# Performance work log

Hardware: AMD Instinct MI355X
Metric: run time of the kernel (lower is better)

Reference implementation:

```python
import jax, jax.numpy as jnp
import numpy as np

N_NODES = 50000
N_EDGES = 600000
N_RELS = 19
D_IN = 128
D_HID = 64
D_OUT = 2


def setup_inputs() -> dict:
    key = jax.random.key(0)
    ks = jax.random.split(key, 10)
    feat = jax.random.normal(ks[0], (N_NODES, D_IN), dtype=jnp.float32)
    src = jax.random.randint(ks[1], (N_EDGES,), 0, N_NODES)
    dst = jax.random.randint(ks[2], (N_EDGES,), 0, N_NODES)
    etype = jax.random.randint(ks[3], (N_EDGES,), 0, N_RELS)
    s1 = 1.0 / np.sqrt(D_IN)
    s2 = 1.0 / np.sqrt(D_HID)
    W1 = jax.random.normal(ks[4], (N_RELS, D_IN, D_HID), dtype=jnp.float32) * s1
    loop1 = jax.random.normal(ks[5], (D_IN, D_HID), dtype=jnp.float32) * s1
    b1 = jnp.zeros((D_HID,), dtype=jnp.float32)
    W2 = jax.random.normal(ks[6], (N_RELS, D_HID, D_OUT), dtype=jnp.float32) * s2
    loop2 = jax.random.normal(ks[7], (D_HID, D_OUT), dtype=jnp.float32) * s2
    b2 = jnp.zeros((D_OUT,), dtype=jnp.float32)
    return {"feat": feat, "W1": W1, "loop1": loop1, "b1": b1,
            "W2": W2, "loop2": loop2, "b2": b2,
            "src": src, "dst": dst, "etype": etype}


def _rel_graph_conv(h, W, loop_w, bias, src, dst, etype, activation):
    # Per-relation transform of all nodes: [N, R, O]; then gather per edge.
    # (num_rels * out_feat is small, so this is cheaper than gathering W per edge.)
    transformed = jnp.einsum('nd,rdo->nro', h, W)
    msg = transformed[src, etype]                      # [E, O] edge messages
    agg = jax.ops.segment_sum(msg, dst, num_segments=h.shape[0])  # scatter-add
    out = agg + h @ loop_w + bias                      # self-loop + bias
    if activation is not None:
        out = activation(out)
    return out


def reference(feat, W1, loop1, b1, W2, loop2, b2, src, dst, etype):
    h = _rel_graph_conv(feat, W1, loop1, b1, src, dst, etype, jax.nn.relu)
    h = _rel_graph_conv(h, W2, loop2, b2, src, dst, etype, None)
    return h
```

## Files before the change

kernel.cpp:

```cpp
#include <hip/hip_runtime.h>

#define N_NODES 50000
#define N_EDGES 600000
#define N_RELS  19
#define D_IN    128
#define D_HID   64
#define D_OUT   2

typedef unsigned short u16;
typedef unsigned int   u32;
typedef __attribute__((ext_vector_type(8))) short sfrag;
typedef __attribute__((ext_vector_type(4))) float f32x4;

__device__ __forceinline__ u16 f2bf(float f){
  union { float f; u32 i; } v; v.f = f;
  u32 r = v.i + 0x7fffu + ((v.i >> 16) & 1u);
  return (u16)(r >> 16);
}

__global__ void k_prep(const float* __restrict__ W1, const float* __restrict__ loop1,
                       const float* __restrict__ W2,
                       u16* __restrict__ W1Tb, u16* __restrict__ loop1Tb,
                       u16* __restrict__ W2Tb){
  int idx = blockIdx.x * 256 + threadIdx.x;
  const int T1 = N_RELS * D_HID * D_IN;
  const int T2 = T1 + N_RELS * 16 * D_HID;
  const int T3 = T2 + D_HID * D_IN;
  if (idx < T1) {
    int r = idx / (D_HID * D_IN);
    int t = idx - r * (D_HID * D_IN);
    int j = t >> 7, d = t & 127;
    W1Tb[idx] = f2bf(W1[(r * D_IN + d) * D_HID + j]);
  } else if (idx < T2) {
    int k2 = idx - T1;
    int r = k2 / (16 * D_HID);
    int t = k2 - r * (16 * D_HID);
    int n = t >> 6, k = t & 63;
    W2Tb[k2] = (n < D_OUT) ? f2bf(W2[(r * D_HID + k) * D_OUT + n]) : (u16)0;
  } else if (idx < T3) {
    int k2 = idx - T2;
    int j = k2 >> 7, d = k2 & 127;
    loop1Tb[k2] = f2bf(loop1[d * D_HID + j]);
  }
}

__global__ void k_zero(int* __restrict__ hist){
  if (threadIdx.x < N_RELS) hist[threadIdx.x] = 0;
}

__global__ __launch_bounds__(256) void k_hist(const int* __restrict__ et, int* __restrict__ hist){
  __shared__ int lh[N_RELS];
  int tid = threadIdx.x;
  if (tid < N_RELS) lh[tid] = 0;
  __syncthreads();
  int e = blockIdx.x * 256 + tid;
  if (e < N_EDGES) atomicAdd(&lh[et[e]], 1);
  __syncthreads();
  if (tid < N_RELS && lh[tid]) atomicAdd(&hist[tid], lh[tid]);
}

__global__ void k_scan(const int* __restrict__ hist, int* __restrict__ offs,
                       int* __restrict__ toff, int* __restrict__ cursor){
  if (threadIdx.x == 0) {
    int acc = 0, tacc = 0;
    offs[0] = 0; toff[0] = 0;
    for (int r = 0; r < N_RELS; ++r) {
      cursor[r] = acc;
      int c = hist[r];
      acc += c;               offs[r + 1] = acc;
      tacc += (c + 63) >> 6;  toff[r + 1] = tacc;
    }
  }
}

__global__ __launch_bounds__(256) void k_scatter(const int* __restrict__ et,
                                                 int* __restrict__ cursor,
                                                 int* __restrict__ perm){
  __shared__ int lh[N_RELS], base[N_RELS];
  int tid = threadIdx.x;
  if (tid < N_RELS) lh[tid] = 0;
  __syncthreads();
  int e = blockIdx.x * 256 + tid;
  int r = 0, my = 0;
  bool valid = e < N_EDGES;
  if (valid) { r = et[e]; my = atomicAdd(&lh[r], 1); }
  __syncthreads();
  if (tid < N_RELS && lh[tid]) base[tid] = atomicAdd(&cursor[tid], lh[tid]);
  __syncthreads();
  if (valid) perm[base[r] + my] = e;
}

__global__ __launch_bounds__(256) void k_selfloop1_mfma(
    const float* __restrict__ feat, const u16* __restrict__ loop1Tb,
    const float* __restrict__ b1, float* __restrict__ agg1){
  __shared__ __align__(16) u16 Als[64][136];
  __shared__ __align__(16) u16 Bls[64][136];
  int tid = threadIdx.x;
  int base = blockIdx.x * 64;
  {
    int j = tid >> 2, seg = tid & 3;
    const uint4* g = (const uint4*)(loop1Tb + j * 128) + seg * 4;
    uint4* d = (uint4*)&Bls[j][seg * 32];
    d[0] = g[0]; d[1] = g[1]; d[2] = g[2]; d[3] = g[3];
  }
  {
    int i = tid >> 2, seg = tid & 3;
    int n = base + i; if (n >= N_NODES) n = 0;
    const float4* fp = (const float4*)(feat + n * D_IN) + seg * 8;
    #pragma unroll
    for (int q = 0; q < 4; ++q) {
      float4 x = fp[2 * q], y = fp[2 * q + 1];
      u32 p0 = (u32)f2bf(x.x) | ((u32)f2bf(x.y) << 16);
      u32 p1 = (u32)f2bf(x.z) | ((u32)f2bf(x.w) << 16);
      u32 p2 = (u32)f2bf(y.x) | ((u32)f2bf(y.y) << 16);
      u32 p3 = (u32)f2bf(y.z) | ((u32)f2bf(y.w) << 16);
      *(uint4*)&Als[i][seg * 32 + q * 8] = make_uint4(p0, p1, p2, p3);
    }
  }
  __syncthreads();

  int w = tid >> 6, lane = tid & 63;
  int r16 = lane & 15, c4 = lane >> 4;
  sfrag aF[4];
  #pragma unroll
  for (int kk = 0; kk < 4; ++kk)
    aF[kk] = *(const sfrag*)&Als[w * 16 + r16][kk * 32 + c4 * 8];
  #pragma unroll
  for (int ct = 0; ct < 4; ++ct) {
    f32x4 acc = {0.f, 0.f, 0.f, 0.f};
    #pragma unroll
    for (int kk = 0; kk < 4; ++kk) {
      sfrag bF = *(const sfrag*)&Bls[ct * 16 + r16][kk * 32 + c4 * 8];
      acc = __builtin_amdgcn_mfma_f32_16x16x32_bf16(aF[kk], bF, acc, 0, 0, 0);
    }
    int col = ct * 16 + r16;
    float bias = b1[col];
    #pragma unroll
    for (int reg = 0; reg < 4; ++reg) {
      int row = base + w * 16 + c4 * 4 + reg;
      if (row < N_NODES) agg1[row * D_HID + col] = acc[reg] + bias;
    }
  }
}

__global__ __launch_bounds__(256) void k_edge1_mfma(
    const float* __restrict__ feat, const u16* __restrict__ W1Tb,
    const int* __restrict__ src, const int* __restrict__ dst,
    const int* __restrict__ perm, const int* __restrict__ offs,
    const int* __restrict__ toff, float* __restrict__ agg1){
  __shared__ __align__(16) u16 Als[64][136];
  __shared__ __align__(16) u16 Bls[64][136];
  __shared__ int dstIds[64];
  __shared__ int sMeta[3];
  int tid = threadIdx.x;
  if (tid == 0) {
    int b = blockIdx.x, r = 0, vc = 0, ts = 0;
    if (b < toff[N_RELS]) {
      while (b >= toff[r + 1]) ++r;
      ts = offs[r] + ((b - toff[r]) << 6);
      vc = offs[r + 1] - ts; if (vc > 64) vc = 64;
    }
    sMeta[0] = r; sMeta[1] = ts; sMeta[2] = vc;
  }
  __syncthreads();
  int vcount = sMeta[2];
  if (vcount == 0) return;
  int rel = sMeta[0], tileStart = sMeta[1];

  {
    int j = tid >> 2, seg = tid & 3;
    const uint4* g = (const uint4*)(W1Tb + (rel * 64 + j) * 128) + seg * 4;
    uint4* d = (uint4*)&Bls[j][seg * 32];
    d[0] = g[0]; d[1] = g[1]; d[2] = g[2]; d[3] = g[3];
  }
  {
    int i = tid >> 2, seg = tid & 3;
    if (i < vcount) {
      int e = perm[tileStart + i];
      if (seg == 0) dstIds[i] = dst[e];
      const float4* fp = (const float4*)(feat + src[e] * D_IN) + seg * 8;
      #pragma unroll
      for (int q = 0; q < 4; ++q) {
        float4 x = fp[2 * q], y = fp[2 * q + 1];
        u32 p0 = (u32)f2bf(x.x) | ((u32)f2bf(x.y) << 16);
        u32 p1 = (u32)f2bf(x.z) | ((u32)f2bf(x.w) << 16);
        u32 p2 = (u32)f2bf(y.x) | ((u32)f2bf(y.y) << 16);
        u32 p3 = (u32)f2bf(y.z) | ((u32)f2bf(y.w) << 16);
        *(uint4*)&Als[i][seg * 32 + q * 8] = make_uint4(p0, p1, p2, p3);
      }
    } else {
      if (seg == 0) dstIds[i] = -1;
      uint4 z = make_uint4(0, 0, 0, 0);
      #pragma unroll
      for (int q = 0; q < 4; ++q) *(uint4*)&Als[i][seg * 32 + q * 8] = z;
    }
  }
  __syncthreads();

  int w = tid >> 6, lane = tid & 63;
  int r16 = lane & 15, c4 = lane >> 4;
  sfrag aF[4];
  #pragma unroll
  for (int kk = 0; kk < 4; ++kk)
    aF[kk] = *(const sfrag*)&Als[w * 16 + r16][kk * 32 + c4 * 8];
  #pragma unroll
  for (int ct = 0; ct < 4; ++ct) {
    f32x4 acc = {0.f, 0.f, 0.f, 0.f};
    #pragma unroll
    for (int kk = 0; kk < 4; ++kk) {
      sfrag bF = *(const sfrag*)&Bls[ct * 16 + r16][kk * 32 + c4 * 8];
      acc = __builtin_amdgcn_mfma_f32_16x16x32_bf16(aF[kk], bF, acc, 0, 0, 0);
    }
    int col = ct * 16 + r16;
    #pragma unroll
    for (int reg = 0; reg < 4; ++reg) {
      int row = w * 16 + c4 * 4 + reg;
      int dn = dstIds[row];
      if (dn >= 0) atomicAdd(&agg1[dn * D_HID + col], acc[reg]);
    }
  }
}

__global__ __launch_bounds__(256) void k_relu_self2(float* __restrict__ agg1,
                                                     const float* __restrict__ loop2,
                                                     const float* __restrict__ b2,
                                                     float* __restrict__ out){
  int wave = threadIdx.x >> 6, lane = threadIdx.x & 63;
  int n = blockIdx.x * 4 + wave;
  float v = agg1[n * D_HID + lane];
  v = v > 0.f ? v : 0.f;
  ((u16*)agg1)[n * D_HID + lane] = f2bf(v);
  float2 lw = ((const float2*)loop2)[lane];
  float p0 = v * lw.x, p1 = v * lw.y;
  for (int off = 32; off; off >>= 1) {
    p0 += __shfl_down(p0, off);
    p1 += __shfl_down(p1, off);
  }
  if (lane == 0) {
    out[n * 2]     = p0 + b2[0];
    out[n * 2 + 1] = p1 + b2[1];
  }
}

__global__ __launch_bounds__(256) void k_edge2_mfma(
    const u16* __restrict__ h1b, const u16* __restrict__ W2Tb,
    const int* __restrict__ src, const int* __restrict__ dst,
    const int* __restrict__ perm, const int* __restrict__ offs,
    const int* __restrict__ toff, float* __restrict__ out){
  __shared__ __align__(16) u16 Als[64][72];
  __shared__ __align__(16) u16 Bls[16][72];
  __shared__ int dstIds[64];
  __shared__ int sMeta[3];
  int tid = threadIdx.x;
  if (tid == 0) {
    int b = blockIdx.x, r = 0, vc = 0, ts = 0;
    if (b < toff[N_RELS]) {
      while (b >= toff[r + 1]) ++r;
      ts = offs[r] + ((b - toff[r]) << 6);
      vc = offs[r + 1] - ts; if (vc > 64) vc = 64;
    }
    sMeta[0] = r; sMeta[1] = ts; sMeta[2] = vc;
  }
  __syncthreads();
  int vcount = sMeta[2];
  if (vcount == 0) return;
  int rel = sMeta[0], tileStart = sMeta[1];

  if (tid < 128) {
    int n = tid >> 3, q = tid & 7;
    ((uint4*)&Bls[n][0])[q] = ((const uint4*)(W2Tb + rel * 16 * 64))[tid];
  }
  {
    int i = tid >> 2, seg = tid & 3;
    if (i < vcount) {
      int e = perm[tileStart + i];
      if (seg == 0) dstIds[i] = dst[e];
      const uint4* g = (const uint4*)(h1b + src[e] * D_HID) + seg * 2;
      *(uint4*)&Als[i][seg * 16]     = g[0];
      *(uint4*)&Als[i][seg * 16 + 8] = g[1];
    } else {
      if (seg == 0) dstIds[i] = -1;
      uint4 z = make_uint4(0, 0, 0, 0);
      *(uint4*)&Als[i][seg * 16]     = z;
      *(uint4*)&Als[i][seg * 16 + 8] = z;
    }
  }
  __syncthreads();

  int w = tid >> 6, lane = tid & 63;
  int r16 = lane & 15, c4 = lane >> 4;
  f32x4 acc = {0.f, 0.f, 0.f, 0.f};
  #pragma unroll
  for (int kk = 0; kk < 2; ++kk) {
    sfrag aF = *(const sfrag*)&Als[w * 16 + r16][kk * 32 + c4 * 8];
    sfrag bF = *(const sfrag*)&Bls[r16][kk * 32 + c4 * 8];
    acc = __builtin_amdgcn_mfma_f32_16x16x32_bf16(aF, bF, acc, 0, 0, 0);
  }
  if (r16 < D_OUT) {
    #pragma unroll
    for (int reg = 0; reg < 4; ++reg) {
      int row = w * 16 + c4 * 4 + reg;
      int dn = dstIds[row];
      if (dn >= 0) atomicAdd(&out[dn * D_OUT + r16], acc[reg]);
    }
  }
}

extern "C" void kernel_launch(void* const* d_in, const int* in_sizes, int n_in,
                              void* d_out, int out_size, void* d_ws, size_t ws_size,
                              hipStream_t stream){
  const float* feat  = (const float*)d_in[0];
  const float* W1    = (const float*)d_in[1];
  const float* loop1 = (const float*)d_in[2];
  const float* b1    = (const float*)d_in[3];
  const float* W2    = (const float*)d_in[4];
  const float* loop2 = (const float*)d_in[5];
  const float* b2    = (const float*)d_in[6];
  const int* src     = (const int*)d_in[7];
  const int* dst     = (const int*)d_in[8];
  const int* et      = (const int*)d_in[9];
  float* out = (float*)d_out;

  char* w = (char*)d_ws;
  u16*   W1Tb    = (u16*)(w);
  u16*   W2Tb    = (u16*)(w + 311296);
  u16*   loop1Tb = (u16*)(w + 350208);
  int*   hist    = (int*)(w + 382976);
  int*   cursor  = (int*)(w + 383104);
  int*   offs    = (int*)(w + 383232);
  int*   toff    = (int*)(w + 383360);
  int*   perm    = (int*)(w + 383488);
  float* agg1    = (float*)(w + 2783488);

  const int MAX_TILES = (N_EDGES + 63) / 64 + N_RELS;

  k_prep          <<<716,   256, 0, stream>>>(W1, loop1, W2, W1Tb, loop1Tb, W2Tb);
  k_zero          <<<1,      64, 0, stream>>>(hist);
  k_hist          <<<2344,  256, 0, stream>>>(et, hist);
  k_scan          <<<1,      64, 0, stream>>>(hist, offs, toff, cursor);
  k_scatter       <<<2344,  256, 0, stream>>>(et, cursor, perm);
  k_selfloop1_mfma<<<(N_NODES + 63) / 64, 256, 0, stream>>>(feat, loop1Tb, b1, agg1);
  k_edge1_mfma    <<<MAX_TILES,   256, 0, stream>>>(feat, W1Tb, src, dst, perm, offs, toff, agg1);
  k_relu_self2    <<<N_NODES / 4, 256, 0, stream>>>(agg1, loop2, b2, out);
  k_edge2_mfma    <<<MAX_TILES,   256, 0, stream>>>((const u16*)agg1, W2Tb, src, dst, perm, offs, toff, out);
}
```

Measured before the change: 337.0 us.

## Pre-convert features to bf16 and accumulate layer-1 scatter with packed bf16 atomics

Adds a kernel that converts the whole feature matrix to bf16 once, so the self-loop and edge kernels gather half as many bytes and skip per-edge conversion. The layer-1 aggregation buffer becomes bf16, and the edge scatter pairs adjacent columns through a lane shuffle and issues global_atomic_pk_add_bf16, halving atomic count and bytes. The cost is an extra full pass over the features and accumulating in bf16, which loses precision when many edges sum into one node.

Result: no change. 336.2 us (-0.3%).

```diff
diff --git a/kernel.cpp b/kernel.cpp
--- a/kernel.cpp
+++ b/kernel.cpp
@@ -16,6 +16,16 @@
   union { float f; u32 i; } v; v.f = f;
   u32 r = v.i + 0x7fffu + ((v.i >> 16) & 1u);
   return (u16)(r >> 16);
+}
+__device__ __forceinline__ float bf2f(u16 u){
+  union { u32 i; float f; } v; v.i = ((u32)u) << 16; return v.f;
+}
+
+__global__ __launch_bounds__(256) void k_featb(const float* __restrict__ feat,
+                                               u16* __restrict__ featb){
+  int i = blockIdx.x * 256 + threadIdx.x;
+  float2 f = ((const float2*)feat)[i];
+  ((u32*)featb)[i] = (u32)f2bf(f.x) | ((u32)f2bf(f.y) << 16);
 }
 
 __global__ void k_prep(const float* __restrict__ W1, const float* __restrict__ loop1,
@@ -91,8 +101,8 @@
 }
 
 __global__ __launch_bounds__(256) void k_selfloop1_mfma(
-    const float* __restrict__ feat, const u16* __restrict__ loop1Tb,
-    const float* __restrict__ b1, float* __restrict__ agg1){
+    const u16* __restrict__ featb, const u16* __restrict__ loop1Tb,
+    const float* __restrict__ b1, u16* __restrict__ agg1b){
   __shared__ __align__(16) u16 Als[64][136];
   __shared__ __align__(16) u16 Bls[64][136];
   int tid = threadIdx.x;
@@ -105,17 +115,10 @@
   }
   {
     int i = tid >> 2, seg = tid & 3;
-    int n = base + i; if (n >= N_NODES) n = 0;
-    const float4* fp = (const float4*)(feat + n * D_IN) + seg * 8;
-    #pragma unroll
-    for (int q = 0; q < 4; ++q) {
-      float4 x = fp[2 * q], y = fp[2 * q + 1];
-      u32 p0 = (u32)f2bf(x.x) | ((u32)f2bf(x.y) << 16);
-      u32 p1 = (u32)f2bf(x.z) | ((u32)f2bf(x.w) << 16);
-      u32 p2 = (u32)f2bf(y.x) | ((u32)f2bf(y.y) << 16);
-      u32 p3 = (u32)f2bf(y.z) | ((u32)f2bf(y.w) << 16);
-      *(uint4*)&Als[i][seg * 32 + q * 8] = make_uint4(p0, p1, p2, p3);
-    }
+    int n = base + i; if (n >= N_NODES) n = N_NODES - 1;
+    const uint4* g = (const uint4*)(featb + n * D_IN) + seg * 4;
+    uint4* d = (uint4*)&Als[i][seg * 32];
+    d[0] = g[0]; d[1] = g[1]; d[2] = g[2]; d[3] = g[3];
   }
   __syncthreads();
 
@@ -138,16 +141,16 @@
     #pragma unroll
     for (int reg = 0; reg < 4; ++reg) {
       int row = base + w * 16 + c4 * 4 + reg;
-      if (row < N_NODES) agg1[row * D_HID + col] = acc[reg] + bias;
+      if (row < N_NODES) agg1b[row * D_HID + col] = f2bf(acc[reg] + bias);
     }
   }
 }
 
 __global__ __launch_bounds__(256) void k_edge1_mfma(
-    const float* __restrict__ feat, const u16* __restrict__ W1Tb,
+    const u16* __restrict__ featb, const u16* __restrict__ W1Tb,
     const int* __restrict__ src, const int* __restrict__ dst,
     const int* __restrict__ perm, const int* __restrict__ offs,
-    const int* __restrict__ toff, float* __restrict__ agg1){
+    const int* __restrict__ toff, u16* __restrict__ agg1b){
   __shared__ __align__(16) u16 Als[64][136];
   __shared__ __align__(16) u16 Bls[64][136];
   __shared__ int dstIds[64];
@@ -178,21 +181,14 @@
     if (i < vcount) {
       int e = perm[tileStart + i];
       if (seg == 0) dstIds[i] = dst[e];
-      const float4* fp = (const float4*)(feat + src[e] * D_IN) + seg * 8;
-      #pragma unroll
-      for (int q = 0; q < 4; ++q) {
-        float4 x = fp[2 * q], y = fp[2 * q + 1];
-        u32 p0 = (u32)f2bf(x.x) | ((u32)f2bf(x.y) << 16);
-        u32 p1 = (u32)f2bf(x.z) | ((u32)f2bf(x.w) << 16);
-        u32 p2 = (u32)f2bf(y.x) | ((u32)f2bf(y.y) << 16);
-        u32 p3 = (u32)f2bf(y.z) | ((u32)f2bf(y.w) << 16);
-        *(uint4*)&Als[i][seg * 32 + q * 8] = make_uint4(p0, p1, p2, p3);
-      }
+      const uint4* g = (const uint4*)(featb + src[e] * D_IN) + seg * 4;
+      uint4* d = (uint4*)&Als[i][seg * 32];
+      d[0] = g[0]; d[1] = g[1]; d[2] = g[2]; d[3] = g[3];
     } else {
       if (seg == 0) dstIds[i] = -1;
       uint4 z = make_uint4(0, 0, 0, 0);
-      #pragma unroll
-      for (int q = 0; q < 4; ++q) *(uint4*)&Als[i][seg * 32 + q * 8] = z;
+      uint4* d = (uint4*)&Als[i][seg * 32];
+      d[0] = z; d[1] = z; d[2] = z; d[3] = z;
     }
   }
   __syncthreads();
@@ -214,22 +210,33 @@
     int col = ct * 16 + r16;
     #pragma unroll
     for (int reg = 0; reg < 4; ++reg) {
-      int row = w * 16 + c4 * 4 + reg;
-      int dn = dstIds[row];
-      if (dn >= 0) atomicAdd(&agg1[dn * D_HID + col], acc[reg]);
-    }
-  }
-}
-
-__global__ __launch_bounds__(256) void k_relu_self2(float* __restrict__ agg1,
+      float other = __shfl_xor(acc[reg], 1);
+      if (!(r16 & 1)) {
+        int row = w * 16 + c4 * 4 + reg;
+        int dn = dstIds[row];
+        if (dn >= 0) {
+          u32 p = (u32)f2bf(acc[reg]) | ((u32)f2bf(other) << 16);
+          unsigned long long a = (unsigned long long)(agg1b + dn * D_HID + col);
+          asm volatile("global_atomic_pk_add_bf16 %0, %1, off"
+                       :: "v"(a), "v"(p) : "memory");
+        }
+      }
+    }
+  }
+  asm volatile("s_waitcnt vmcnt(0)" ::: "memory");
+}
+
+__global__ __launch_bounds__(256) void k_relu_self2(u16* __restrict__ agg1b,
                                                      const float* __restrict__ loop2,
                                                      const float* __restrict__ b2,
                                                      float* __restrict__ out){
   int wave = threadIdx.x >> 6, lane = threadIdx.x & 63;
   int n = blockIdx.x * 4 + wave;
-  float v = agg1[n * D_HID + lane];
-  v = v > 0.f ? v : 0.f;
-  ((u16*)agg1)[n * D_HID + lane] = f2bf(v);
+  u16 u = agg1b[n * D_HID + lane];
+  float v = bf2f(u);
+  bool neg = v <= 0.f;
+  if (neg) v = 0.f;
+  agg1b[n * D_HID + lane] = neg ? (u16)0 : u;
   float2 lw = ((const float2*)loop2)[lane];
   float p0 = v * lw.x, p1 = v * lw.y;
   for (int off = 32; off; off >>= 1) {
@@ -330,17 +337,19 @@
   int*   offs    = (int*)(w + 383232);
   int*   toff    = (int*)(w + 383360);
   int*   perm    = (int*)(w + 383488);
-  float* agg1    = (float*)(w + 2783488);
+  u16*   featb   = (u16*)(w + 2783488);
+  u16*   agg1b   = (u16*)(w + 15583488);
 
   const int MAX_TILES = (N_EDGES + 63) / 64 + N_RELS;
 
   k_prep          <<<716,   256, 0, stream>>>(W1, loop1, W2, W1Tb, loop1Tb, W2Tb);
+  k_featb         <<<12500, 256, 0, stream>>>(feat, featb);
   k_zero          <<<1,      64, 0, stream>>>(hist);
   k_hist          <<<2344,  256, 0, stream>>>(et, hist);
   k_scan          <<<1,      64, 0, stream>>>(hist, offs, toff, cursor);
   k_scatter       <<<2344,  256, 0, stream>>>(et, cursor, perm);
-  k_selfloop1_mfma<<<(N_NODES + 63) / 64, 256, 0, stream>>>(feat, loop1Tb, b1, agg1);
-  k_edge1_mfma    <<<MAX_TILES,   256, 0, stream>>>(feat, W1Tb, src, dst, perm, offs, toff, agg1);
-  k_relu_self2    <<<N_NODES / 4, 256, 0, stream>>>(agg1, loop2, b2, out);
-  k_edge2_mfma    <<<MAX_TILES,   256, 0, stream>>>((const u16*)agg1, W2Tb, src, dst, perm, offs, toff, out);
-}
+  k_selfloop1_mfma<<<(N_NODES + 63) / 64, 256, 0, stream>>>(featb, loop1Tb, b1, agg1b);
+  k_edge1_mfma    <<<MAX_TILES,   256, 0, stream>>>(featb, W1Tb, src, dst, perm, offs, toff, agg1b);
+  k_relu_self2    <<<N_NODES / 4, 256, 0, stream>>>(agg1b, loop2, b2, out);
+  k_edge2_mfma    <<<MAX_TILES,   256, 0, stream>>>(agg1b, W2Tb, src, dst, perm, offs, toff, out);
+}
```
